# Kernel tuning notes

Measured on AMD Instinct MI355X. Metric: run time of the kernel, lower is better.

## Reference

```python
import jax, jax.numpy as jnp
import numpy as np

B, M, N = 1, 8192, 131072      # batch, bones, window points
C_BOT, C = 16, 128             # bottleneck_channel, channel
K_MAX, FOLD, R_UP = 8, 8, 4    # max neighbors, fold_channel, upsample rate r
EPS = 1e-8


def _lin_init(key, fan_in, fan_out):
    return jax.random.normal(key, (fan_in, fan_out), jnp.float32) / np.sqrt(fan_in)


def setup_inputs() -> dict:
    key = jax.random.key(0)
    ks = jax.random.split(key, 10)
    return {
        "quantized_cf": jax.random.normal(ks[0], (B, M, C_BOT), jnp.float32),
        "d_idx": jax.random.randint(ks[1], (B, N, K_MAX), 0, M),
        "d_windows": jax.random.normal(ks[2], (B, N, 3), jnp.float32),
        "bones": jax.random.normal(ks[3], (B, M, 3), jnp.float32),
        "K": 8,
        # fea_stretch Linear(bottleneck -> channel)
        "W_stretch": _lin_init(ks[4], C_BOT, C),
        "b_stretch": jnp.zeros((C,), jnp.float32),
        # DWUS folding MLP: (C+3) -> C -> FOLD*R_UP -> 3 (per fold point)
        "W1": _lin_init(ks[5], C + 3, C),
        "b1": jnp.zeros((C,), jnp.float32),
        "W2": _lin_init(ks[6], C, FOLD * R_UP),
        "b2": jnp.zeros((FOLD * R_UP,), jnp.float32),
        "W3": _lin_init(ks[7], FOLD, 3),
        "b3": jnp.zeros((3,), jnp.float32),
    }


def reference(quantized_cf, d_idx, d_windows, bones, K,
              W_stretch, b_stretch, W1, b1, W2, b2, W3, b3):
    # fea_stretch: per-bone feature expansion  [B, M, C]
    skin_fea = jnp.einsum("bmc,cd->bmd", quantized_cf, W_stretch) + b_stretch

    idx = d_idx[..., :K]                                   # [B, N, K]
    batch = jnp.arange(B)[:, None, None]
    g_fea = skin_fea[batch, idx]                           # [B, N, K, C] gather
    g_bones = bones[batch, idx]                            # [B, N, K, 3]

    # inverse-distance interpolation of bone features onto window points
    rel = d_windows[:, :, None, :] - g_bones               # [B, N, K, 3]
    dist = jnp.sqrt(jnp.sum(rel * rel, axis=-1) + EPS)     # [B, N, K]
    w = 1.0 / (dist + EPS)
    w = w / jnp.sum(w, axis=-1, keepdims=True)
    interp = jnp.einsum("bnk,bnkc->bnc", w, g_fea)         # [B, N, C]

    # folding-based upsampling: each window point emits R_UP refined points
    x = jnp.concatenate([interp, d_windows], axis=-1)      # [B, N, C+3]
    h = jax.nn.relu(jnp.einsum("bnc,cd->bnd", x, W1) + b1)
    h = jax.nn.relu(jnp.einsum("bnc,cd->bnd", h, W2) + b2)
    h = h.reshape(B, N, R_UP, FOLD)
    off = jnp.einsum("bnrf,fo->bnro", h, W3) + b3          # [B, N, R_UP, 3]
    rec = d_windows[:, :, None, :] + off                   # [B, N, R_UP, 3]
    return rec.reshape(B, N * R_UP, 3)
```

## Files before the change

kernel.cpp:

```cpp
#include <hip/hip_runtime.h>
#include <hip/hip_bf16.h>

typedef __attribute__((ext_vector_type(8))) short short8;
typedef __attribute__((ext_vector_type(4))) float f32x4;

#define NPTS 131072

__device__ inline unsigned short f2bf(float f) {
    unsigned u = __float_as_uint(f);
    u = (u + 0x7FFFu + ((u >> 16) & 1u)) >> 16;
    return (unsigned short)u;
}

__device__ inline unsigned pack2(float a, float b) {
    union { __hip_bfloat162 h; unsigned u; } v;
    v.h = __float22bfloat162_rn(float2{a, b});
    return v.u;
}

__global__ __launch_bounds__(256) void prep_kernel(
    const float* __restrict__ Ws, const float* __restrict__ bs,
    const float* __restrict__ W1, const float* __restrict__ b1,
    const float* __restrict__ W2, const float* __restrict__ W3,
    const float* __restrict__ bones,
    unsigned short* __restrict__ w1t, unsigned short* __restrict__ w2t,
    float* __restrict__ beff, unsigned short* __restrict__ w3t,
    float* __restrict__ bones4)
{
    int t = blockIdx.x * 256 + threadIdx.x;
    if (t < 4096) {
        int e = t >> 5, k = t & 31;
        float v = 0.f;
        if (k < 16) {
            for (int d = 0; d < 128; ++d) v = fmaf(Ws[k*128 + d], W1[d*128 + e], v);
        } else if (k < 19) {
            v = W1[(128 + (k - 16))*128 + e];
        }
        w1t[e*32 + k] = f2bf(v);
    } else if (t < 8192) {
        int t2 = t - 4096;
        int e = t2 >> 7, d = t2 & 127;
        w2t[e*128 + ((d & 15)*8 + (d >> 4))] = f2bf(W2[d*32 + e]);
    } else if (t < 8320) {
        int e = t - 8192;
        float v = b1[e];
        for (int d = 0; d < 128; ++d) v = fmaf(bs[d], W1[d*128 + e], v);
        beff[e] = v;
    } else if (t < 8832) {
        int i = t - 8320;
        int q = i >> 5, k = i & 31;
        int e = (k & 1)*16 + (k >> 1);
        int r = e >> 3, f = e & 7;
        float v = 0.f;
        if (q < 12) {
            int r2 = q / 3, o = q - r2*3;
            if (r == r2) v = W3[f*3 + o];
        }
        w3t[q*32 + k] = f2bf(v);
    } else if (t < 8832 + 4*8192) {
        int i = t - 8832;
        int id = i >> 2, c = i & 3;
        bones4[i] = (c < 3) ? bones[id*3 + c] : 0.f;
    }
}

__global__ __launch_bounds__(64, 2) void decoder_kernel(
    const float* __restrict__ qcf, const int* __restrict__ didx,
    const float* __restrict__ dwin, const float* __restrict__ bones4,
    const unsigned short* __restrict__ w1t, const unsigned short* __restrict__ w2t,
    const float* __restrict__ beff, const float* __restrict__ b2,
    const unsigned short* __restrict__ w3t, const float* __restrict__ b3,
    float* __restrict__ out)
{
    __shared__ unsigned short H1b[16 * 136];
    __shared__ unsigned short H2p[16 * 40];

    const int lane = threadIdx.x;
    const int q4   = lane >> 4;
    const int l16  = lane & 15;

    const int base = blockIdx.x * 16;
    const int p    = base + l16;

    short8 W1f[8]; float beffv[8];
#pragma unroll
    for (int dt = 0; dt < 8; ++dt) {
        W1f[dt]   = *(const short8*)(w1t + (dt*16 + l16)*32 + q4*8);
        beffv[dt] = beff[dt*16 + l16];
    }
    short8 W2f[2][4]; float b2v[2];
#pragma unroll
    for (int et = 0; et < 2; ++et) {
        b2v[et] = b2[et*16 + l16];
#pragma unroll
        for (int kt = 0; kt < 4; ++kt)
            W2f[et][kt] = *(const short8*)(w2t + (et*16 + l16)*128 + kt*32 + q4*8);
    }
    const short8 w3f = *(const short8*)(w3t + l16*32 + q4*8);
    const int   o3c  = l16 - (l16/3)*3;
    const float b3o  = (l16 < 12) ? b3[o3c] : 0.f;

    const int4 ia = *(const int4*)(didx + p*8);
    const int4 ib = *(const int4*)(didx + p*8 + 4);
    const int id[8] = { ia.x, ia.y, ia.z, ia.w, ib.x, ib.y, ib.z, ib.w };
    const float wx = dwin[p*3+0], wy = dwin[p*3+1], wz = dwin[p*3+2];

    const float4* __restrict__ bn4 = (const float4*)bones4;
    float w[8]; float s = 0.f;
#pragma unroll
    for (int k = 0; k < 8; ++k) {
        const float4 b = bn4[id[k]];
        const float rx = wx - b.x, ry = wy - b.y, rz = wz - b.z;
        const float dist = sqrtf(fmaf(rx,rx, fmaf(ry,ry, fmaf(rz,rz, 1e-8f))));
        w[k] = 1.0f / (dist + 1e-8f);
        s += w[k];
    }
    const float inv = 1.0f / s;

    union { unsigned u[4]; short8 s8; } a1u;
    a1u.u[0] = a1u.u[1] = a1u.u[2] = a1u.u[3] = 0u;
    if (q4 < 2) {
        float acc[8] = {0.f,0.f,0.f,0.f,0.f,0.f,0.f,0.f};
        const float4* __restrict__ q4p = (const float4*)qcf;
#pragma unroll
        for (int k = 0; k < 8; ++k) {
            const float4 lo = q4p[id[k]*4 + q4*2 + 0];
            const float4 hi = q4p[id[k]*4 + q4*2 + 1];
            acc[0] = fmaf(w[k], lo.x, acc[0]);
            acc[1] = fmaf(w[k], lo.y, acc[1]);
            acc[2] = fmaf(w[k], lo.z, acc[2]);
            acc[3] = fmaf(w[k], lo.w, acc[3]);
            acc[4] = fmaf(w[k], hi.x, acc[4]);
            acc[5] = fmaf(w[k], hi.y, acc[5]);
            acc[6] = fmaf(w[k], hi.z, acc[6]);
            acc[7] = fmaf(w[k], hi.w, acc[7]);
        }
        a1u.u[0] = pack2(acc[0]*inv, acc[1]*inv);
        a1u.u[1] = pack2(acc[2]*inv, acc[3]*inv);
        a1u.u[2] = pack2(acc[4]*inv, acc[5]*inv);
        a1u.u[3] = pack2(acc[6]*inv, acc[7]*inv);
    } else if (q4 == 2) {
        a1u.u[0] = pack2(wx, wy);
        a1u.u[1] = pack2(wz, 0.f);
    }

    f32x4 acc1[8];
#pragma unroll
    for (int dt = 0; dt < 8; ++dt) {
        f32x4 c = { beffv[dt], beffv[dt], beffv[dt], beffv[dt] };
        acc1[dt] = __builtin_amdgcn_mfma_f32_16x16x32_bf16(a1u.s8, W1f[dt], c, 0, 0, 0);
    }
#pragma unroll
    for (int r = 0; r < 4; ++r) {
        union { unsigned u[4]; short8 s8; } pk;
        pk.u[0] = pack2(fmaxf(acc1[0][r],0.f), fmaxf(acc1[1][r],0.f));
        pk.u[1] = pack2(fmaxf(acc1[2][r],0.f), fmaxf(acc1[3][r],0.f));
        pk.u[2] = pack2(fmaxf(acc1[4][r],0.f), fmaxf(acc1[5][r],0.f));
        pk.u[3] = pack2(fmaxf(acc1[6][r],0.f), fmaxf(acc1[7][r],0.f));
        *(short8*)(H1b + (q4*4 + r)*136 + l16*8) = pk.s8;
    }
    __syncthreads();

    f32x4 acc2[2] = { { b2v[0], b2v[0], b2v[0], b2v[0] },
                      { b2v[1], b2v[1], b2v[1], b2v[1] } };
#pragma unroll
    for (int kt = 0; kt < 4; ++kt) {
        const short8 a2 = *(const short8*)(H1b + l16*136 + kt*32 + q4*8);
        acc2[0] = __builtin_amdgcn_mfma_f32_16x16x32_bf16(a2, W2f[0][kt], acc2[0], 0, 0, 0);
        acc2[1] = __builtin_amdgcn_mfma_f32_16x16x32_bf16(a2, W2f[1][kt], acc2[1], 0, 0, 0);
    }
#pragma unroll
    for (int r = 0; r < 4; ++r) {
        unsigned p01 = pack2(fmaxf(acc2[0][r],0.f), fmaxf(acc2[1][r],0.f));
        *(unsigned*)(H2p + (q4*4 + r)*40 + l16*2) = p01;
    }
    __syncthreads();

    const short8 a3 = *(const short8*)(H2p + l16*40 + q4*8);
    f32x4 c3 = { b3o, b3o, b3o, b3o };
    f32x4 o3 = __builtin_amdgcn_mfma_f32_16x16x32_bf16(a3, w3f, c3, 0, 0, 0);
    if (l16 < 12) {
#pragma unroll
        for (int r = 0; r < 4; ++r) {
            const int pt = base + q4*4 + r;
            out[(size_t)pt*12 + l16] = dwin[pt*3 + o3c] + o3[r];
        }
    }
}

extern "C" void kernel_launch(void* const* d_in, const int* in_sizes, int n_in,
                              void* d_out, int out_size, void* d_ws, size_t ws_size,
                              hipStream_t stream) {
    const float* qcf   = (const float*)d_in[0];
    const int*   didx  = (const int*)  d_in[1];
    const float* dwin  = (const float*)d_in[2];
    const float* bones = (const float*)d_in[3];
    const float* Ws = (const float*)d_in[5];
    const float* bs = (const float*)d_in[6];
    const float* W1 = (const float*)d_in[7];
    const float* b1 = (const float*)d_in[8];
    const float* W2 = (const float*)d_in[9];
    const float* b2 = (const float*)d_in[10];
    const float* W3 = (const float*)d_in[11];
    const float* b3 = (const float*)d_in[12];
    float* out = (float*)d_out;

    unsigned short* w1t    = (unsigned short*)d_ws;
    unsigned short* w2t    = (unsigned short*)((char*)d_ws + 8192);
    float*          beff   = (float*)((char*)d_ws + 16384);
    unsigned short* w3t    = (unsigned short*)((char*)d_ws + 16896);
    float*          bones4 = (float*)((char*)d_ws + 17920);

    hipLaunchKernelGGL(prep_kernel, dim3(163), dim3(256), 0, stream,
                       Ws, bs, W1, b1, W2, W3, bones, w1t, w2t, beff, w3t, bones4);
    hipLaunchKernelGGL(decoder_kernel, dim3(NPTS/16), dim3(64), 0, stream,
                       qcf, didx, dwin, bones4, w1t, w2t, beff, b2, w3t, b3, out);
}
```

Baseline: 38.73 us.

## Split gather/interpolation into separate kernel writing bf16 MLP input buffer

Splits the fused decoder into a gather kernel, which computes inverse-distance weights and the interpolated bottleneck features per point and writes them as a packed bf16 row, and an MLP kernel that reads that row as the MFMA A operand. The aim is to keep the latency-bound random gathers out of the MFMA kernel and give them full 256-thread occupancy. In exchange it adds an extra kernel launch and a 64-byte-per-point round trip through global memory. It also drops the two-blocks-per-CU launch bound, prefetches the window coordinates early in the MLP kernel, and adds unroll pragmas to the prep loops.

```diff
diff --git a/kernel.cpp b/kernel.cpp
--- a/kernel.cpp
+++ b/kernel.cpp
@@ -32,6 +32,7 @@
         int e = t >> 5, k = t & 31;
         float v = 0.f;
         if (k < 16) {
+#pragma unroll 16
             for (int d = 0; d < 128; ++d) v = fmaf(Ws[k*128 + d], W1[d*128 + e], v);
         } else if (k < 19) {
             v = W1[(128 + (k - 16))*128 + e];
@@ -44,6 +45,7 @@
     } else if (t < 8320) {
         int e = t - 8192;
         float v = b1[e];
+#pragma unroll 16
         for (int d = 0; d < 128; ++d) v = fmaf(bs[d], W1[d*128 + e], v);
         beff[e] = v;
     } else if (t < 8832) {
@@ -64,9 +66,60 @@
     }
 }
 
-__global__ __launch_bounds__(64, 2) void decoder_kernel(
+__global__ __launch_bounds__(256) void gather_kernel(
     const float* __restrict__ qcf, const int* __restrict__ didx,
     const float* __restrict__ dwin, const float* __restrict__ bones4,
+    unsigned* __restrict__ X)
+{
+    const int p = blockIdx.x * 256 + threadIdx.x;
+    const int4 ia = *(const int4*)(didx + p*8);
+    const int4 ib = *(const int4*)(didx + p*8 + 4);
+    const int id[8] = { ia.x, ia.y, ia.z, ia.w, ib.x, ib.y, ib.z, ib.w };
+    const float wx = dwin[p*3+0], wy = dwin[p*3+1], wz = dwin[p*3+2];
+
+    const float4* __restrict__ bn4 = (const float4*)bones4;
+    float w[8]; float s = 0.f;
+#pragma unroll
+    for (int k = 0; k < 8; ++k) {
+        const float4 b = bn4[id[k]];
+        const float rx = wx - b.x, ry = wy - b.y, rz = wz - b.z;
+        const float dist = sqrtf(fmaf(rx,rx, fmaf(ry,ry, fmaf(rz,rz, 1e-8f))));
+        w[k] = 1.0f / (dist + 1e-8f);
+        s += w[k];
+    }
+    const float inv = 1.0f / s;
+
+    float4 a0 = {0,0,0,0}, a1 = {0,0,0,0}, a2 = {0,0,0,0}, a3 = {0,0,0,0};
+#pragma unroll
+    for (int k = 0; k < 8; ++k) {
+        const float4* __restrict__ q = (const float4*)(qcf + id[k]*16);
+        const float4 q0 = q[0], q1 = q[1], q2 = q[2], q3 = q[3];
+        const float wk = w[k];
+        a0.x = fmaf(wk, q0.x, a0.x); a0.y = fmaf(wk, q0.y, a0.y);
+        a0.z = fmaf(wk, q0.z, a0.z); a0.w = fmaf(wk, q0.w, a0.w);
+        a1.x = fmaf(wk, q1.x, a1.x); a1.y = fmaf(wk, q1.y, a1.y);
+        a1.z = fmaf(wk, q1.z, a1.z); a1.w = fmaf(wk, q1.w, a1.w);
+        a2.x = fmaf(wk, q2.x, a2.x); a2.y = fmaf(wk, q2.y, a2.y);
+        a2.z = fmaf(wk, q2.z, a2.z); a2.w = fmaf(wk, q2.w, a2.w);
+        a3.x = fmaf(wk, q3.x, a3.x); a3.y = fmaf(wk, q3.y, a3.y);
+        a3.z = fmaf(wk, q3.z, a3.z); a3.w = fmaf(wk, q3.w, a3.w);
+    }
+
+    uint4 o0, o1, o2, o3;
+    o0.x = pack2(a0.x*inv, a0.y*inv); o0.y = pack2(a0.z*inv, a0.w*inv);
+    o0.z = pack2(a1.x*inv, a1.y*inv); o0.w = pack2(a1.z*inv, a1.w*inv);
+    o1.x = pack2(a2.x*inv, a2.y*inv); o1.y = pack2(a2.z*inv, a2.w*inv);
+    o1.z = pack2(a3.x*inv, a3.y*inv); o1.w = pack2(a3.z*inv, a3.w*inv);
+    o2.x = pack2(wx, wy);             o2.y = pack2(wz, 0.f);
+    o2.z = 0u; o2.w = 0u;
+    o3.x = 0u; o3.y = 0u; o3.z = 0u; o3.w = 0u;
+
+    uint4* __restrict__ xp = (uint4*)(X + (size_t)p * 16);
+    xp[0] = o0; xp[1] = o1; xp[2] = o2; xp[3] = o3;
+}
+
+__global__ __launch_bounds__(64) void mlp_kernel(
+    const unsigned* __restrict__ X, const float* __restrict__ dwin,
     const unsigned short* __restrict__ w1t, const unsigned short* __restrict__ w2t,
     const float* __restrict__ beff, const float* __restrict__ b2,
     const unsigned short* __restrict__ w3t, const float* __restrict__ b3,
@@ -78,9 +131,19 @@
     const int lane = threadIdx.x;
     const int q4   = lane >> 4;
     const int l16  = lane & 15;
-
-    const int base = blockIdx.x * 16;
-    const int p    = base + l16;
+    const int tbase = blockIdx.x * 16;
+
+    union { uint4 v; short8 s8; } xa;
+    xa.v = *(const uint4*)(X + (size_t)(tbase + l16) * 16 + q4*4);
+
+    const int o3c = l16 - (l16/3)*3;
+    float rw0 = 0.f, rw1 = 0.f, rw2 = 0.f, rw3 = 0.f;
+    if (l16 < 12) {
+        rw0 = dwin[(size_t)(tbase + q4*4 + 0)*3 + o3c];
+        rw1 = dwin[(size_t)(tbase + q4*4 + 1)*3 + o3c];
+        rw2 = dwin[(size_t)(tbase + q4*4 + 2)*3 + o3c];
+        rw3 = dwin[(size_t)(tbase + q4*4 + 3)*3 + o3c];
+    }
 
     short8 W1f[8]; float beffv[8];
 #pragma unroll
@@ -97,58 +160,13 @@
             W2f[et][kt] = *(const short8*)(w2t + (et*16 + l16)*128 + kt*32 + q4*8);
     }
     const short8 w3f = *(const short8*)(w3t + l16*32 + q4*8);
-    const int   o3c  = l16 - (l16/3)*3;
-    const float b3o  = (l16 < 12) ? b3[o3c] : 0.f;
-
-    const int4 ia = *(const int4*)(didx + p*8);
-    const int4 ib = *(const int4*)(didx + p*8 + 4);
-    const int id[8] = { ia.x, ia.y, ia.z, ia.w, ib.x, ib.y, ib.z, ib.w };
-    const float wx = dwin[p*3+0], wy = dwin[p*3+1], wz = dwin[p*3+2];
-
-    const float4* __restrict__ bn4 = (const float4*)bones4;
-    float w[8]; float s = 0.f;
-#pragma unroll
-    for (int k = 0; k < 8; ++k) {
-        const float4 b = bn4[id[k]];
-        const float rx = wx - b.x, ry = wy - b.y, rz = wz - b.z;
-        const float dist = sqrtf(fmaf(rx,rx, fmaf(ry,ry, fmaf(rz,rz, 1e-8f))));
-        w[k] = 1.0f / (dist + 1e-8f);
-        s += w[k];
-    }
-    const float inv = 1.0f / s;
-
-    union { unsigned u[4]; short8 s8; } a1u;
-    a1u.u[0] = a1u.u[1] = a1u.u[2] = a1u.u[3] = 0u;
-    if (q4 < 2) {
-        float acc[8] = {0.f,0.f,0.f,0.f,0.f,0.f,0.f,0.f};
-        const float4* __restrict__ q4p = (const float4*)qcf;
-#pragma unroll
-        for (int k = 0; k < 8; ++k) {
-            const float4 lo = q4p[id[k]*4 + q4*2 + 0];
-            const float4 hi = q4p[id[k]*4 + q4*2 + 1];
-            acc[0] = fmaf(w[k], lo.x, acc[0]);
-            acc[1] = fmaf(w[k], lo.y, acc[1]);
-            acc[2] = fmaf(w[k], lo.z, acc[2]);
-            acc[3] = fmaf(w[k], lo.w, acc[3]);
-            acc[4] = fmaf(w[k], hi.x, acc[4]);
-            acc[5] = fmaf(w[k], hi.y, acc[5]);
-            acc[6] = fmaf(w[k], hi.z, acc[6]);
-            acc[7] = fmaf(w[k], hi.w, acc[7]);
-        }
-        a1u.u[0] = pack2(acc[0]*inv, acc[1]*inv);
-        a1u.u[1] = pack2(acc[2]*inv, acc[3]*inv);
-        a1u.u[2] = pack2(acc[4]*inv, acc[5]*inv);
-        a1u.u[3] = pack2(acc[6]*inv, acc[7]*inv);
-    } else if (q4 == 2) {
-        a1u.u[0] = pack2(wx, wy);
-        a1u.u[1] = pack2(wz, 0.f);
-    }
+    const float  b3o = (l16 < 12) ? b3[o3c] : 0.f;
 
     f32x4 acc1[8];
 #pragma unroll
     for (int dt = 0; dt < 8; ++dt) {
         f32x4 c = { beffv[dt], beffv[dt], beffv[dt], beffv[dt] };
-        acc1[dt] = __builtin_amdgcn_mfma_f32_16x16x32_bf16(a1u.s8, W1f[dt], c, 0, 0, 0);
+        acc1[dt] = __builtin_amdgcn_mfma_f32_16x16x32_bf16(xa.s8, W1f[dt], c, 0, 0, 0);
     }
 #pragma unroll
     for (int r = 0; r < 4; ++r) {
@@ -180,11 +198,10 @@
     f32x4 c3 = { b3o, b3o, b3o, b3o };
     f32x4 o3 = __builtin_amdgcn_mfma_f32_16x16x32_bf16(a3, w3f, c3, 0, 0, 0);
     if (l16 < 12) {
-#pragma unroll
-        for (int r = 0; r < 4; ++r) {
-            const int pt = base + q4*4 + r;
-            out[(size_t)pt*12 + l16] = dwin[pt*3 + o3c] + o3[r];
-        }
+        out[(size_t)(tbase + q4*4 + 0)*12 + l16] = rw0 + o3[0];
+        out[(size_t)(tbase + q4*4 + 1)*12 + l16] = rw1 + o3[1];
+        out[(size_t)(tbase + q4*4 + 2)*12 + l16] = rw2 + o3[2];
+        out[(size_t)(tbase + q4*4 + 3)*12 + l16] = rw3 + o3[3];
     }
 }
 
@@ -210,9 +227,12 @@
     float*          beff   = (float*)((char*)d_ws + 16384);
     unsigned short* w3t    = (unsigned short*)((char*)d_ws + 16896);
     float*          bones4 = (float*)((char*)d_ws + 17920);
+    unsigned*       X      = (unsigned*)((char*)d_ws + (1u<<20));
 
     hipLaunchKernelGGL(prep_kernel, dim3(163), dim3(256), 0, stream,
                        Ws, bs, W1, b1, W2, W3, bones, w1t, w2t, beff, w3t, bones4);
-    hipLaunchKernelGGL(decoder_kernel, dim3(NPTS/16), dim3(64), 0, stream,
-                       qcf, didx, dwin, bones4, w1t, w2t, beff, b2, w3t, b3, out);
-}
+    hipLaunchKernelGGL(gather_kernel, dim3(NPTS/256), dim3(256), 0, stream,
+                       qcf, didx, dwin, bones4, X);
+    hipLaunchKernelGGL(mlp_kernel, dim3(NPTS/16), dim3(64), 0, stream,
+                       X, dwin, w1t, w2t, beff, b2, w3t, b3, out);
+}
```

Result: slower. 49.11 us (+26.8%).

## Pack four independent waves per block and defer weight loads past gather

Applied to the files above, without the earlier changes.

Blocks now hold four waves, each processing its own 16-point tile with a private LDS region, giving 2048 blocks of 256 threads instead of 8192 single-wave blocks. Launch bounds change to allow 3 blocks per CU. Weight fragment loads move after the gather and interpolation to shorten register live ranges. The output residual window values are prefetched early to hide that load latency. The syncthreads now stall all four waves together even though they share no data, which may add barrier cost.

```diff
diff --git a/kernel.cpp b/kernel.cpp
--- a/kernel.cpp
+++ b/kernel.cpp
@@ -64,7 +64,9 @@
     }
 }
 
-__global__ __launch_bounds__(64, 2) void decoder_kernel(
+#define WREG 5632
+
+__global__ __launch_bounds__(256, 3) void decoder_kernel(
     const float* __restrict__ qcf, const int* __restrict__ didx,
     const float* __restrict__ dwin, const float* __restrict__ bones4,
     const unsigned short* __restrict__ w1t, const unsigned short* __restrict__ w2t,
@@ -72,38 +74,35 @@
     const unsigned short* __restrict__ w3t, const float* __restrict__ b3,
     float* __restrict__ out)
 {
-    __shared__ unsigned short H1b[16 * 136];
-    __shared__ unsigned short H2p[16 * 40];
-
-    const int lane = threadIdx.x;
-    const int q4   = lane >> 4;
-    const int l16  = lane & 15;
-
-    const int base = blockIdx.x * 16;
+    __shared__ unsigned char lds[4 * WREG];
+
+    const int tid  = threadIdx.x;
+    const int wave = tid >> 6;
+    const int lane = tid & 63;
+    unsigned char* wbase = lds + wave * WREG;
+    unsigned short* H1b = (unsigned short*)(wbase);
+    unsigned short* H2p = (unsigned short*)(wbase + 4352);
+
+    const int q4  = lane >> 4;
+    const int l16 = lane & 15;
+
+    const int gw   = blockIdx.x * 4 + wave;
+    const int base = gw * 16;
     const int p    = base + l16;
-
-    short8 W1f[8]; float beffv[8];
-#pragma unroll
-    for (int dt = 0; dt < 8; ++dt) {
-        W1f[dt]   = *(const short8*)(w1t + (dt*16 + l16)*32 + q4*8);
-        beffv[dt] = beff[dt*16 + l16];
-    }
-    short8 W2f[2][4]; float b2v[2];
-#pragma unroll
-    for (int et = 0; et < 2; ++et) {
-        b2v[et] = b2[et*16 + l16];
-#pragma unroll
-        for (int kt = 0; kt < 4; ++kt)
-            W2f[et][kt] = *(const short8*)(w2t + (et*16 + l16)*128 + kt*32 + q4*8);
-    }
-    const short8 w3f = *(const short8*)(w3t + l16*32 + q4*8);
-    const int   o3c  = l16 - (l16/3)*3;
-    const float b3o  = (l16 < 12) ? b3[o3c] : 0.f;
 
     const int4 ia = *(const int4*)(didx + p*8);
     const int4 ib = *(const int4*)(didx + p*8 + 4);
     const int id[8] = { ia.x, ia.y, ia.z, ia.w, ib.x, ib.y, ib.z, ib.w };
     const float wx = dwin[p*3+0], wy = dwin[p*3+1], wz = dwin[p*3+2];
+
+    const int o3c = l16 - (l16/3)*3;
+    float rw0 = 0.f, rw1 = 0.f, rw2 = 0.f, rw3 = 0.f;
+    if (l16 < 12) {
+        rw0 = dwin[(size_t)(base + q4*4 + 0)*3 + o3c];
+        rw1 = dwin[(size_t)(base + q4*4 + 1)*3 + o3c];
+        rw2 = dwin[(size_t)(base + q4*4 + 2)*3 + o3c];
+        rw3 = dwin[(size_t)(base + q4*4 + 3)*3 + o3c];
+    }
 
     const float4* __restrict__ bn4 = (const float4*)bones4;
     float w[8]; float s = 0.f;
@@ -144,6 +143,23 @@
         a1u.u[1] = pack2(wz, 0.f);
     }
 
+    short8 W1f[8]; float beffv[8];
+#pragma unroll
+    for (int dt = 0; dt < 8; ++dt) {
+        W1f[dt]   = *(const short8*)(w1t + (dt*16 + l16)*32 + q4*8);
+        beffv[dt] = beff[dt*16 + l16];
+    }
+    short8 W2f[2][4]; float b2v[2];
+#pragma unroll
+    for (int et = 0; et < 2; ++et) {
+        b2v[et] = b2[et*16 + l16];
+#pragma unroll
+        for (int kt = 0; kt < 4; ++kt)
+            W2f[et][kt] = *(const short8*)(w2t + (et*16 + l16)*128 + kt*32 + q4*8);
+    }
+    const short8 w3f = *(const short8*)(w3t + l16*32 + q4*8);
+    const float  b3o = (l16 < 12) ? b3[o3c] : 0.f;
+
     f32x4 acc1[8];
 #pragma unroll
     for (int dt = 0; dt < 8; ++dt) {
@@ -180,11 +196,10 @@
     f32x4 c3 = { b3o, b3o, b3o, b3o };
     f32x4 o3 = __builtin_amdgcn_mfma_f32_16x16x32_bf16(a3, w3f, c3, 0, 0, 0);
     if (l16 < 12) {
-#pragma unroll
-        for (int r = 0; r < 4; ++r) {
-            const int pt = base + q4*4 + r;
-            out[(size_t)pt*12 + l16] = dwin[pt*3 + o3c] + o3[r];
-        }
+        out[(size_t)(base + q4*4 + 0)*12 + l16] = rw0 + o3[0];
+        out[(size_t)(base + q4*4 + 1)*12 + l16] = rw1 + o3[1];
+        out[(size_t)(base + q4*4 + 2)*12 + l16] = rw2 + o3[2];
+        out[(size_t)(base + q4*4 + 3)*12 + l16] = rw3 + o3[3];
     }
 }
 
@@ -213,6 +228,6 @@
 
     hipLaunchKernelGGL(prep_kernel, dim3(163), dim3(256), 0, stream,
                        Ws, bs, W1, b1, W2, W3, bones, w1t, w2t, beff, w3t, bones4);
-    hipLaunchKernelGGL(decoder_kernel, dim3(NPTS/16), dim3(64), 0, stream,
+    hipLaunchKernelGGL(decoder_kernel, dim3(2048), dim3(256), 0, stream,
                        qcf, didx, dwin, bones4, w1t, w2t, beff, b2, w3t, b3, out);
 }
```

After: 35.19 us. 1.1x faster.
